# Kernel optimization log

Measured on AMD Instinct MI355X. Metric: run time of the kernel, lower is better.

The kernel has to match this reference:

```python
import jax, jax.numpy as jnp
import numpy as np

N_NODES = 100000
N_EDGES = 1600000
D_IN = 128
D_HID = 128
N_CLS = 40


def setup_inputs() -> dict:
    key = jax.random.key(0)
    ks = jax.random.split(key, 8)
    x = jax.random.normal(ks[0], (N_NODES, D_IN), dtype=jnp.float32)
    edge_index = jax.random.randint(ks[1], (2, N_EDGES), 0, N_NODES, dtype=jnp.int64)
    s = 1.0 / np.sqrt(D_IN)
    W1_l = jax.random.normal(ks[2], (D_IN, D_HID), dtype=jnp.float32) * s
    W1_r = jax.random.normal(ks[3], (D_IN, D_HID), dtype=jnp.float32) * s
    b1 = jnp.zeros((D_HID,), dtype=jnp.float32)
    s2 = 1.0 / np.sqrt(D_HID)
    W2_l = jax.random.normal(ks[4], (D_HID, N_CLS), dtype=jnp.float32) * s2
    W2_r = jax.random.normal(ks[5], (D_HID, N_CLS), dtype=jnp.float32) * s2
    b2 = jnp.zeros((N_CLS,), dtype=jnp.float32)
    return {"x": x, "edge_index": edge_index, "W1_l": W1_l, "W1_r": W1_r,
            "b1": b1, "W2_l": W2_l, "W2_r": W2_r, "b2": b2}


def _sage_conv(x, src, dst, Wl, Wr, b):
    # mean-aggregate neighbor features (PyG SAGEConv, aggr='mean')
    n = x.shape[0]
    agg = jax.ops.segment_sum(x[src], dst, num_segments=n)           # [N, d]
    deg = jax.ops.segment_sum(jnp.ones_like(dst, dtype=x.dtype), dst, num_segments=n)
    mean = agg / jnp.maximum(deg, 1.0)[:, None]
    # lin_l(mean) + bias + lin_r(x_root)  (lin_r has no bias in PyG)
    return mean @ Wl + b + x @ Wr


def reference(x, edge_index, W1_l, W1_r, b1, W2_l, W2_r, b2):
    src, dst = edge_index[0], edge_index[1]
    h = jax.nn.relu(_sage_conv(x, src, dst, W1_l, W1_r, b1))
    # F.dropout(training=...) is identity in eval mode (deterministic reference)
    out = _sage_conv(h, src, dst, W2_l, W2_r, b2)
    return jax.nn.softmax(out, axis=1)
```

## Files before the change

kernel.cpp:

```cpp
#include <hip/hip_runtime.h>

#define DIM 128
#define NCLS 40
#define CPAD 64
#define NBIN 256
#define BINSH 9
#define CHUNK 4096

typedef unsigned short ushort_t;
typedef __attribute__((ext_vector_type(8))) short bf16x8;
typedef __attribute__((ext_vector_type(4))) float f32x4;
typedef __attribute__((ext_vector_type(4))) unsigned uint4a;

__device__ __forceinline__ ushort_t f2b(float f) {
    union { float f; unsigned u; } v; v.f = f;
    unsigned r = v.u + 0x7FFFu + ((v.u >> 16) & 1u);
    return (ushort_t)(r >> 16);
}

__device__ __forceinline__ float b2f(ushort_t b) {
    union { unsigned u; float f; } v; v.u = ((unsigned)b) << 16;
    return v.f;
}

__device__ __forceinline__ void acc_fp8x4(float4& a, int w) {
    a.x += __builtin_amdgcn_cvt_f32_fp8(w, 0);
    a.y += __builtin_amdgcn_cvt_f32_fp8(w, 1);
    a.z += __builtin_amdgcn_cvt_f32_fp8(w, 2);
    a.w += __builtin_amdgcn_cvt_f32_fp8(w, 3);
}

__device__ __forceinline__ void acc_pair(float& a, float& b, unsigned u) {
    union { unsigned x; float f; } lo, hi;
    lo.x = u << 16;
    hi.x = u & 0xFFFF0000u;
    a += lo.f;
    b += hi.f;
}

__device__ __forceinline__ void acc_row40(float* lg, uint4a v0, uint4a v1,
                                          uint4a v2, uint4a v3, uint4a v4) {
    acc_pair(lg[0],  lg[1],  v0.x); acc_pair(lg[2],  lg[3],  v0.y);
    acc_pair(lg[4],  lg[5],  v0.z); acc_pair(lg[6],  lg[7],  v0.w);
    acc_pair(lg[8],  lg[9],  v1.x); acc_pair(lg[10], lg[11], v1.y);
    acc_pair(lg[12], lg[13], v1.z); acc_pair(lg[14], lg[15], v1.w);
    acc_pair(lg[16], lg[17], v2.x); acc_pair(lg[18], lg[19], v2.y);
    acc_pair(lg[20], lg[21], v2.z); acc_pair(lg[22], lg[23], v2.w);
    acc_pair(lg[24], lg[25], v3.x); acc_pair(lg[26], lg[27], v3.y);
    acc_pair(lg[28], lg[29], v3.z); acc_pair(lg[30], lg[31], v3.w);
    acc_pair(lg[32], lg[33], v4.x); acc_pair(lg[34], lg[35], v4.y);
    acc_pair(lg[36], lg[37], v4.z); acc_pair(lg[38], lg[39], v4.w);
}

__global__ __launch_bounds__(256) void prep_kernel(
    const float* __restrict__ x, ushort_t* __restrict__ xbf, unsigned* __restrict__ xq,
    const float* __restrict__ W1r, const float* __restrict__ W1l, ushort_t* __restrict__ Wp,
    const float* __restrict__ W2l, ushort_t* __restrict__ Wp2,
    const float* __restrict__ W2r, ushort_t* __restrict__ Wp2r,
    int* __restrict__ binCnt, int* __restrict__ binCtr, int n4, int cb)
{
    const int b = blockIdx.x;
    if (b < cb) {
        int i = b * 256 + threadIdx.x;
        if (i >= n4) return;
        f32x4 v = __builtin_nontemporal_load(((const f32x4*)x) + i);
        ushort4 o;
        o.x = f2b(v.x); o.y = f2b(v.y); o.z = f2b(v.z); o.w = f2b(v.w);
        ((ushort4*)xbf)[i] = o;
        int p = __builtin_amdgcn_cvt_pk_fp8_f32(v.x, v.y, 0, false);
        p = __builtin_amdgcn_cvt_pk_fp8_f32(v.z, v.w, p, true);
        xq[i] = (unsigned)p;
    } else if (b < cb + 128) {
        int o = (b - cb) * 256 + threadIdx.x;
        int j    = o & 7;
        int lane = (o >> 3) & 63;
        int t    = (o >> 9) & 7;
        int kc   = o >> 12;
        int k = kc * 32 + (lane >> 4) * 8 + j;
        int nn = t * 16 + (lane & 15);
        float v = (k < DIM) ? W1r[k * DIM + nn] : W1l[(k - DIM) * DIM + nn];
        Wp[o] = f2b(v);
    } else if (b < cb + 152) {
        int o = (b - cb - 128) * 256 + threadIdx.x;
        int j    = o & 7;
        int lane = (o >> 3) & 63;
        int rem  = o >> 9;
        int t    = rem % 3;
        int kc   = rem / 3;
        int k  = kc * 32 + (lane >> 4) * 8 + j;
        int nn = t * 16 + (lane & 15);
        Wp2[o] = (nn < NCLS) ? f2b(W2l[k * NCLS + nn]) : (ushort_t)0;
    } else if (b < cb + 176) {
        int o = (b - cb - 152) * 256 + threadIdx.x;
        int j    = o & 7;
        int lane = (o >> 3) & 63;
        int rem  = o >> 9;
        int t    = rem % 3;
        int kc   = rem / 3;
        int k  = kc * 32 + (lane >> 4) * 8 + j;
        int nn = t * 16 + (lane & 15);
        Wp2r[o] = (nn < NCLS) ? f2b(W2r[k * NCLS + nn]) : (ushort_t)0;
    } else {
        binCnt[threadIdx.x] = 0;
        binCtr[threadIdx.x] = 0;
    }
}


__global__ __launch_bounds__(256) void bincount_kernel(const int* __restrict__ dst,
                                                       int* __restrict__ binCnt, int E) {
    __shared__ int hist[NBIN];
    hist[threadIdx.x] = 0;
    __syncthreads();
    const int tid = blockIdx.x * 256 + threadIdx.x;
    const int stride = gridDim.x * 256;
    for (int e = tid; e < E; e += stride)
        atomicAdd(&hist[__builtin_nontemporal_load(dst + e) >> BINSH], 1);
    __syncthreads();
    if (hist[threadIdx.x]) atomicAdd(&binCnt[threadIdx.x], hist[threadIdx.x]);
}

__global__ __launch_bounds__(256) void binscatter_kernel(
    const int* __restrict__ src, const int* __restrict__ dst,
    const int* __restrict__ binCnt, int* __restrict__ binCtr,
    unsigned* __restrict__ pairs, int E)
{
    __shared__ int ss[CHUNK];
    __shared__ int sd[CHUNK];
    __shared__ int excl[NBIN];
    __shared__ int hist[NBIN];
    __shared__ int base[NBIN];
    __shared__ int cnt[NBIN];
    const int t = threadIdx.x;
    excl[t] = binCnt[t];
    __syncthreads();
    for (int off = 1; off < NBIN; off <<= 1) {
        int v = (t >= off) ? excl[t - off] : 0;
        __syncthreads();
        excl[t] += v;
        __syncthreads();
    }
    const int mybase = (t == 0) ? 0 : excl[t - 1];
    __syncthreads();
    excl[t] = mybase;
    __syncthreads();
    const int nchunk = (E + CHUNK - 1) / CHUNK;
    for (int c = blockIdx.x; c < nchunk; c += gridDim.x) {
        const int e0 = c * CHUNK;
        const int m = min(CHUNK, E - e0);
        for (int i = t; i < m; i += 256) {
            ss[i] = __builtin_nontemporal_load(src + e0 + i);
            sd[i] = __builtin_nontemporal_load(dst + e0 + i);
        }
        hist[t] = 0;
        cnt[t] = 0;
        __syncthreads();
        for (int i = t; i < m; i += 256)
            atomicAdd(&hist[sd[i] >> BINSH], 1);
        __syncthreads();
        base[t] = hist[t] ? (excl[t] + atomicAdd(&binCtr[t], hist[t])) : 0;
        __syncthreads();
        for (int i = t; i < m; i += 256) {
            int d = sd[i];
            int b = d >> BINSH;
            int off = base[b] + atomicAdd(&cnt[b], 1);
            pairs[off] = ((unsigned)(d & ((1 << BINSH) - 1)) << 17) | (unsigned)ss[i];
        }
        __syncthreads();
    }
}

__global__ __launch_bounds__(256) void bincsr_kernel(
    const unsigned* __restrict__ pairs, const int* __restrict__ binCnt,
    int* __restrict__ row_ptr, int* __restrict__ eidx, int n, int E)
{
    __shared__ int bs[NBIN];
    __shared__ int deg[512];
    __shared__ int sc[512];
    __shared__ int cnt[512];
    const int b  = blockIdx.x;
    const int t = threadIdx.x;
    bs[t] = binCnt[t];
    __syncthreads();
    for (int off = 1; off < NBIN; off <<= 1) {
        int v = (t >= off) ? bs[t - off] : 0;
        __syncthreads();
        bs[t] += v;
        __syncthreads();
    }
    const int lo = (b == 0) ? 0 : bs[b - 1];
    const int hi = bs[b];
    const int nlo = b << BINSH;
    deg[t] = 0; deg[t + 256] = 0;
    cnt[t] = 0; cnt[t + 256] = 0;
    __syncthreads();
    for (int e = lo + t; e < hi; e += 256)
        atomicAdd(&deg[pairs[e] >> 17], 1);
    __syncthreads();
    sc[t] = deg[t];
    sc[t + 256] = deg[t + 256];
    __syncthreads();
    for (int off = 1; off < 512; off <<= 1) {
        int v0 = (t >= off) ? sc[t - off] : 0;
        int v1 = sc[t + 256 - off];
        __syncthreads();
        sc[t] += v0;
        sc[t + 256] += v1;
        __syncthreads();
    }
    {
        int node0 = nlo + t;
        int node1 = nlo + t + 256;
        if (node0 < n) row_ptr[node0] = lo + sc[t] - deg[t];
        if (node1 < n) row_ptr[node1] = lo + sc[t + 256] - deg[t + 256];
    }
    if (b == NBIN - 1 && t == 255) row_ptr[n] = E;
    for (int e = lo + t; e < hi; e += 256) {
        unsigned p = pairs[e];
        int dl = p >> 17;
        int slot = sc[dl] - deg[dl] + atomicAdd(&cnt[dl], 1);
        eidx[lo + slot] = (int)(p & 0x1FFFFu);
    }
}


__global__ __launch_bounds__(256) void gather128_kernel(
    const unsigned* __restrict__ xq, const int* __restrict__ row_ptr,
    const int* __restrict__ eidx, ushort_t* __restrict__ Bbf, int n)
{
    int t = blockIdx.x * 256 + threadIdx.x;
    int node = t >> 5;
    if (node >= n) return;
    int q = t & 31;
    int j  = row_ptr[node];
    int je = row_ptr[node + 1];
    const float id = 1.0f / fmaxf((float)(je - j), 1.0f);
    float4 acc = make_float4(0.f, 0.f, 0.f, 0.f);
    for (; j + 3 < je; j += 4) {
        int s0 = eidx[j], s1 = eidx[j + 1], s2 = eidx[j + 2], s3 = eidx[j + 3];
        int w0 = (int)xq[(size_t)s0 * 32 + q];
        int w1 = (int)xq[(size_t)s1 * 32 + q];
        int w2 = (int)xq[(size_t)s2 * 32 + q];
        int w3 = (int)xq[(size_t)s3 * 32 + q];
        acc_fp8x4(acc, w0); acc_fp8x4(acc, w1);
        acc_fp8x4(acc, w2); acc_fp8x4(acc, w3);
    }
    for (; j < je; ++j) {
        int s0 = eidx[j];
        acc_fp8x4(acc, (int)xq[(size_t)s0 * 32 + q]);
    }
    ushort4 o;
    o.x = f2b(acc.x * id); o.y = f2b(acc.y * id);
    o.z = f2b(acc.z * id); o.w = f2b(acc.w * id);
    ((ushort4*)(Bbf + (size_t)node * DIM))[q] = o;
}

__global__ __launch_bounds__(256) void mfma_gemm_kernel(
    const ushort_t* __restrict__ xbf, const ushort_t* __restrict__ mxbf,
    const ushort_t* __restrict__ Wp, const ushort_t* __restrict__ Wp2,
    const ushort_t* __restrict__ Wp2r, const float* __restrict__ bias,
    ushort_t* __restrict__ Cbf, float* __restrict__ Dfl, int n)
{
    __shared__ ushort_t hl[4][16 * 136];
    const int wave = threadIdx.x >> 6;
    const int lane = threadIdx.x & 63;
    const int m16  = lane & 15;
    const int quad = lane >> 4;
    const int row0 = blockIdx.x * 64 + wave * 16;
    int arow = row0 + m16;
    if (arow >= n) arow = n - 1;
    f32x4 acc[8];
    #pragma unroll
    for (int t = 0; t < 8; ++t) acc[t] = (f32x4){0.f, 0.f, 0.f, 0.f};
    const ushort_t* __restrict__ xrow = xbf  + (size_t)arow * DIM;
    const ushort_t* __restrict__ mrow = mxbf + (size_t)arow * DIM;
    #pragma unroll
    for (int kc = 0; kc < 8; ++kc) {
        const int kcol = (kc & 3) * 32 + quad * 8;
        const bf16x8 afrag = *(const bf16x8*)((kc < 4 ? xrow : mrow) + kcol);
        const ushort_t* __restrict__ wp = Wp + (size_t)kc * 4096 + (size_t)lane * 8;
        #pragma unroll
        for (int t = 0; t < 8; ++t) {
            const bf16x8 bfrag = *(const bf16x8*)(wp + (size_t)t * 512);
            acc[t] = __builtin_amdgcn_mfma_f32_16x16x32_bf16(afrag, bfrag, acc[t], 0, 0, 0);
        }
    }
    ushort_t* __restrict__ hw = hl[wave];
    #pragma unroll
    for (int t = 0; t < 8; ++t) {
        const int col = t * 16 + m16;
        const float bv = bias[col];
        #pragma unroll
        for (int r = 0; r < 4; ++r) {
            hw[(quad * 4 + r) * 136 + col] = f2b(fmaxf(acc[t][r] + bv, 0.f));
        }
    }
    f32x4 acc2[3];
    f32x4 acc3[3];
    #pragma unroll
    for (int t = 0; t < 3; ++t) {
        acc2[t] = (f32x4){0.f, 0.f, 0.f, 0.f};
        acc3[t] = (f32x4){0.f, 0.f, 0.f, 0.f};
    }
    #pragma unroll
    for (int kc = 0; kc < 4; ++kc) {
        const bf16x8 afrag2 = *(const bf16x8*)(hw + m16 * 136 + kc * 32 + quad * 8);
        const ushort_t* __restrict__ wp2  = Wp2  + (size_t)kc * 1536 + (size_t)lane * 8;
        const ushort_t* __restrict__ wp2r = Wp2r + (size_t)kc * 1536 + (size_t)lane * 8;
        #pragma unroll
        for (int t = 0; t < 3; ++t) {
            const bf16x8 bfrag  = *(const bf16x8*)(wp2  + (size_t)t * 512);
            const bf16x8 bfragr = *(const bf16x8*)(wp2r + (size_t)t * 512);
            acc2[t] = __builtin_amdgcn_mfma_f32_16x16x32_bf16(afrag2, bfrag,  acc2[t], 0, 0, 0);
            acc3[t] = __builtin_amdgcn_mfma_f32_16x16x32_bf16(afrag2, bfragr, acc3[t], 0, 0, 0);
        }
    }
    #pragma unroll
    for (int t = 0; t < 3; ++t) {
        const int col = t * 16 + m16;
        if (col >= NCLS) continue;
        #pragma unroll
        for (int r = 0; r < 4; ++r) {
            const int row = row0 + quad * 4 + r;
            if (row < n) {
                Cbf[(size_t)row * CPAD + col] = f2b(acc2[t][r]);
                Dfl[(size_t)row * NCLS + col] = acc3[t][r];
            }
        }
    }
}

__global__ __launch_bounds__(256) void final_kernel(
    const float* __restrict__ Dfl, const ushort_t* __restrict__ Cbf,
    const int* __restrict__ row_ptr, const int* __restrict__ eidx,
    const float* __restrict__ b2,
    float* __restrict__ out, int n)
{
    __shared__ float lgs[64][41];
    const int tid  = threadIdx.x;
    const int q    = tid >> 6;
    const int lane = tid & 63;
    const int r    = lane & 3;
    const int na   = q * 16 + (lane >> 2);
    const int nodeA = blockIdx.x * 64 + na;
    float lg[40];
    #pragma unroll
    for (int c = 0; c < 40; ++c) lg[c] = 0.f;
    if (nodeA < n) {
        int j  = row_ptr[nodeA] + r;
        int je = row_ptr[nodeA + 1];
        for (; j + 4 < je; j += 8) {
            int s0 = eidx[j];
            int s1 = eidx[j + 4];
            const uint4a* __restrict__ p0 = (const uint4a*)(Cbf + (size_t)s0 * CPAD);
            const uint4a* __restrict__ p1 = (const uint4a*)(Cbf + (size_t)s1 * CPAD);
            uint4a a0 = p0[0], a1 = p0[1], a2 = p0[2], a3 = p0[3], a4 = p0[4];
            uint4a c0v = p1[0], c1 = p1[1], c2 = p1[2], c3 = p1[3], c4 = p1[4];
            acc_row40(lg, a0, a1, a2, a3, a4);
            acc_row40(lg, c0v, c1, c2, c3, c4);
        }
        if (j < je) {
            const uint4a* __restrict__ p0 = (const uint4a*)(Cbf + (size_t)eidx[j] * CPAD);
            uint4a a0 = p0[0], a1 = p0[1], a2 = p0[2], a3 = p0[3], a4 = p0[4];
            acc_row40(lg, a0, a1, a2, a3, a4);
        }
    }
    const bool hi1 = (lane & 1) != 0;
    float h20[20];
    #pragma unroll
    for (int i = 0; i < 20; ++i) {
        float sendv = hi1 ? lg[i] : lg[20 + i];
        float recv  = __shfl_xor(sendv, 1, 64);
        h20[i] = (hi1 ? lg[20 + i] : lg[i]) + recv;
    }
    const bool hi2 = (lane & 2) != 0;
    float h10[10];
    #pragma unroll
    for (int i = 0; i < 10; ++i) {
        float sendv = hi2 ? h20[i] : h20[10 + i];
        float recv  = __shfl_xor(sendv, 2, 64);
        h10[i] = (hi2 ? h20[10 + i] : h20[i]) + recv;
    }
    const int cbase = (hi1 ? 20 : 0) + (hi2 ? 10 : 0);
    #pragma unroll
    for (int i = 0; i < 10; ++i) lgs[na][cbase + i] = h10[i];
    __syncthreads();
    const int c0 = __builtin_amdgcn_readfirstlane(q * 10);
    const int node = blockIdx.x * 64 + lane;
    if (node < n) {
        const float dg = (float)(row_ptr[node + 1] - row_ptr[node]);
        const float id = 1.0f / fmaxf(dg, 1.0f);
        const float* __restrict__ drow = Dfl + (size_t)node * NCLS + c0;
        #pragma unroll
        for (int c = 0; c < 10; ++c)
            lgs[lane][c0 + c] = fmaf(lgs[lane][c0 + c], id, b2[c0 + c]) + drow[c];
    }
    __syncthreads();
    if (q == 0 && node < n) {
        float v[NCLS];
        #pragma unroll
        for (int c = 0; c < NCLS; ++c) v[c] = lgs[lane][c];
        float m = v[0];
        #pragma unroll
        for (int c = 1; c < NCLS; ++c) m = fmaxf(m, v[c]);
        float s = 0.f;
        #pragma unroll
        for (int c = 0; c < NCLS; ++c) { v[c] = __expf(v[c] - m); s += v[c]; }
        const float inv = 1.0f / s;
        float* __restrict__ o = out + (size_t)node * NCLS;
        #pragma unroll
        for (int c = 0; c < NCLS; ++c) o[c] = v[c] * inv;
    }
}

extern "C" void kernel_launch(void* const* d_in, const int* in_sizes, int n_in,
                              void* d_out, int out_size, void* d_ws, size_t ws_size,
                              hipStream_t stream) {
    const float* x   = (const float*)d_in[0];
    const int*   ei  = (const int*)d_in[1];
    const float* W1l = (const float*)d_in[2];
    const float* W1r = (const float*)d_in[3];
    const float* b1  = (const float*)d_in[4];
    const float* W2l = (const float*)d_in[5];
    const float* W2r = (const float*)d_in[6];
    const float* b2  = (const float*)d_in[7];
    float* out = (float*)d_out;

    const int n = in_sizes[0] / DIM;
    const int E = in_sizes[1] / 2;
    const int* src = ei;
    const int* dst = ei + E;

    ushort_t* xbf     = (ushort_t*)d_ws;
    ushort_t* mxbf    = xbf + (size_t)n * DIM;
    float*    Dfl     = (float*)(mxbf + (size_t)n * DIM);
    ushort_t* Cbf     = (ushort_t*)(Dfl + (size_t)n * NCLS);
    unsigned* xq      = (unsigned*)(Cbf + (size_t)n * CPAD);
    ushort_t* Wp      = (ushort_t*)(xq + (size_t)n * 32);
    ushort_t* Wp2     = Wp + 256 * DIM;
    ushort_t* Wp2r    = Wp2 + 4 * 1536;
    int*      eidx    = (int*)(Wp2r + 4 * 1536);
    unsigned* pairs   = (unsigned*)(eidx + E);
    int*      row_ptr = (int*)(pairs + E);
    int*      binCnt  = row_ptr + (n + 1);
    int*      binCtr  = binCnt + NBIN;

    const int n4 = n * 32;
    const int cb = (n4 + 255) / 256;
    prep_kernel<<<cb + 177, 256, 0, stream>>>(x, xbf, xq, W1r, W1l, Wp,
                                              W2l, Wp2, W2r, Wp2r,
                                              binCnt, binCtr, n4, cb);

    bincount_kernel  <<<512, 256, 0, stream>>>(dst, binCnt, E);
    binscatter_kernel<<<512, 256, 0, stream>>>(src, dst, binCnt, binCtr, pairs, E);
    bincsr_kernel    <<<NBIN, 256, 0, stream>>>(pairs, binCnt, row_ptr, eidx, n, E);

    {
        long long t = (long long)n * 32;
        gather128_kernel<<<(int)((t + 255) / 256), 256, 0, stream>>>(xq, row_ptr, eidx, mxbf, n);
    }
    mfma_gemm_kernel<<<(n + 63) / 64, 256, 0, stream>>>(xbf, mxbf, Wp, Wp2, Wp2r,
                                                        b1, Cbf, Dfl, n);

    final_kernel<<<(n + 63) / 64, 256, 0, stream>>>(Dfl, Cbf, row_ptr, eidx, b2, out, n);
}
```

Baseline: 289.6 us.

## Fuse bin counting into prep kernel, memset bins, unroll fp8 gather

Folds the edge-destination histogram into extra blocks of the prep kernel so it runs alongside the bf16/fp8 conversion and weight packing. Bin counters are now zeroed with an async memset beforehand. The fp8 gather uses packed two-value conversions and an 8-way unrolled loop so more neighbour loads are in flight. This removes one kernel launch and lets histogram work overlap the conversion, at the cost of an extra memset node and higher register pressure in the gather.

```diff
diff --git a/kernel.cpp b/kernel.cpp
--- a/kernel.cpp
+++ b/kernel.cpp
@@ -10,6 +10,7 @@
 typedef unsigned short ushort_t;
 typedef __attribute__((ext_vector_type(8))) short bf16x8;
 typedef __attribute__((ext_vector_type(4))) float f32x4;
+typedef __attribute__((ext_vector_type(2))) float f32x2;
 typedef __attribute__((ext_vector_type(4))) unsigned uint4a;
 
 __device__ __forceinline__ ushort_t f2b(float f) {
@@ -24,10 +25,9 @@
 }
 
 __device__ __forceinline__ void acc_fp8x4(float4& a, int w) {
-    a.x += __builtin_amdgcn_cvt_f32_fp8(w, 0);
-    a.y += __builtin_amdgcn_cvt_f32_fp8(w, 1);
-    a.z += __builtin_amdgcn_cvt_f32_fp8(w, 2);
-    a.w += __builtin_amdgcn_cvt_f32_fp8(w, 3);
+    f32x2 lo = __builtin_amdgcn_cvt_pk_f32_fp8(w, false);
+    f32x2 hi = __builtin_amdgcn_cvt_pk_f32_fp8(w, true);
+    a.x += lo.x; a.y += lo.y; a.z += hi.x; a.w += hi.y;
 }
 
 __device__ __forceinline__ void acc_pair(float& a, float& b, unsigned u) {
@@ -57,7 +57,7 @@
     const float* __restrict__ W1r, const float* __restrict__ W1l, ushort_t* __restrict__ Wp,
     const float* __restrict__ W2l, ushort_t* __restrict__ Wp2,
     const float* __restrict__ W2r, ushort_t* __restrict__ Wp2r,
-    int* __restrict__ binCnt, int* __restrict__ binCtr, int n4, int cb)
+    const int* __restrict__ dst, int* __restrict__ binCnt, int E, int n4, int cb)
 {
     const int b = blockIdx.x;
     if (b < cb) {
@@ -101,24 +101,20 @@
         int nn = t * 16 + (lane & 15);
         Wp2r[o] = (nn < NCLS) ? f2b(W2r[k * NCLS + nn]) : (ushort_t)0;
     } else {
-        binCnt[threadIdx.x] = 0;
-        binCtr[threadIdx.x] = 0;
-    }
-}
-
-
-__global__ __launch_bounds__(256) void bincount_kernel(const int* __restrict__ dst,
-                                                       int* __restrict__ binCnt, int E) {
-    __shared__ int hist[NBIN];
-    hist[threadIdx.x] = 0;
-    __syncthreads();
-    const int tid = blockIdx.x * 256 + threadIdx.x;
-    const int stride = gridDim.x * 256;
-    for (int e = tid; e < E; e += stride)
-        atomicAdd(&hist[__builtin_nontemporal_load(dst + e) >> BINSH], 1);
-    __syncthreads();
-    if (hist[threadIdx.x]) atomicAdd(&binCnt[threadIdx.x], hist[threadIdx.x]);
-}
+        __shared__ int hist[NBIN];
+        hist[threadIdx.x] = 0;
+        __syncthreads();
+        const int nb = (int)gridDim.x - (cb + 176);
+        const int bi = b - (cb + 176);
+        const int tid = bi * 256 + threadIdx.x;
+        const int stride = nb * 256;
+        for (int e = tid; e < E; e += stride)
+            atomicAdd(&hist[__builtin_nontemporal_load(dst + e) >> BINSH], 1);
+        __syncthreads();
+        if (hist[threadIdx.x]) atomicAdd(&binCnt[threadIdx.x], hist[threadIdx.x]);
+    }
+}
+
 
 __global__ __launch_bounds__(256) void binscatter_kernel(
     const int* __restrict__ src, const int* __restrict__ dst,
@@ -236,6 +232,22 @@
     int je = row_ptr[node + 1];
     const float id = 1.0f / fmaxf((float)(je - j), 1.0f);
     float4 acc = make_float4(0.f, 0.f, 0.f, 0.f);
+    for (; j + 7 < je; j += 8) {
+        int s0 = eidx[j],     s1 = eidx[j + 1], s2 = eidx[j + 2], s3 = eidx[j + 3];
+        int s4 = eidx[j + 4], s5 = eidx[j + 5], s6 = eidx[j + 6], s7 = eidx[j + 7];
+        int w0 = (int)xq[(size_t)s0 * 32 + q];
+        int w1 = (int)xq[(size_t)s1 * 32 + q];
+        int w2 = (int)xq[(size_t)s2 * 32 + q];
+        int w3 = (int)xq[(size_t)s3 * 32 + q];
+        int w4 = (int)xq[(size_t)s4 * 32 + q];
+        int w5 = (int)xq[(size_t)s5 * 32 + q];
+        int w6 = (int)xq[(size_t)s6 * 32 + q];
+        int w7 = (int)xq[(size_t)s7 * 32 + q];
+        acc_fp8x4(acc, w0); acc_fp8x4(acc, w1);
+        acc_fp8x4(acc, w2); acc_fp8x4(acc, w3);
+        acc_fp8x4(acc, w4); acc_fp8x4(acc, w5);
+        acc_fp8x4(acc, w6); acc_fp8x4(acc, w7);
+    }
     for (; j + 3 < je; j += 4) {
         int s0 = eidx[j], s1 = eidx[j + 1], s2 = eidx[j + 2], s3 = eidx[j + 3];
         int w0 = (int)xq[(size_t)s0 * 32 + q];
@@ -443,16 +455,16 @@
     unsigned* pairs   = (unsigned*)(eidx + E);
     int*      row_ptr = (int*)(pairs + E);
     int*      binCnt  = row_ptr + (n + 1);
-    int*      binCtr  = binCnt + NBIN;
+
+    hipMemsetAsync(binCnt, 0, 2 * NBIN * sizeof(int), stream);
 
     const int n4 = n * 32;
     const int cb = (n4 + 255) / 256;
-    prep_kernel<<<cb + 177, 256, 0, stream>>>(x, xbf, xq, W1r, W1l, Wp,
-                                              W2l, Wp2, W2r, Wp2r,
-                                              binCnt, binCtr, n4, cb);
-
-    bincount_kernel  <<<512, 256, 0, stream>>>(dst, binCnt, E);
-    binscatter_kernel<<<512, 256, 0, stream>>>(src, dst, binCnt, binCtr, pairs, E);
+    prep_kernel<<<cb + 176 + 256, 256, 0, stream>>>(x, xbf, xq, W1r, W1l, Wp,
+                                                    W2l, Wp2, W2r, Wp2r,
+                                                    dst, binCnt, E, n4, cb);
+
+    binscatter_kernel<<<512, 256, 0, stream>>>(src, dst, binCnt, binCnt + NBIN, pairs, E);
     bincsr_kernel    <<<NBIN, 256, 0, stream>>>(pairs, binCnt, row_ptr, eidx, n, E);
 
     {
```

After: 282.8 us, median of 2. -2.4%, faster.
